# Kernel optimization log

Measured on AMD Instinct MI355X. Metric: run time of the kernel, lower is better.

Reference implementation:

```python
import jax, jax.numpy as jnp
import numpy as np


def setup_inputs() -> dict:
    key = jax.random.key(0)
    kx, kwi, kwh = jax.random.split(key, 3)
    B, T, F, H = 32, 2048, 512, 512
    x = jax.random.normal(kx, (B, T, F), dtype=jnp.float32)
    c0 = jnp.zeros((B, H), dtype=jnp.float32)
    h0 = jnp.zeros((B, H), dtype=jnp.float32)
    # Flax OptimizedLSTMCell: fused kernels, gates in (i, f, g, o) order.
    # Input projection has no bias; recurrent projection carries the bias.
    Wi = jax.random.normal(kwi, (F, 4 * H), dtype=jnp.float32) / np.sqrt(F)
    Wh = jax.random.normal(kwh, (H, 4 * H), dtype=jnp.float32) / np.sqrt(H)
    b = jnp.zeros((4 * H,), dtype=jnp.float32)
    return {"x": x, "c0": c0, "h0": h0, "Wi": Wi, "Wh": Wh, "b": b}


def reference(x, c0, h0, Wi, Wh, b):
    # x: [B, T, F]; scan over time (axis 1), matching nn.scan(in_axes=1, out_axes=1).
    def step(carry, xt):
        c, h = carry
        z = xt @ Wi + h @ Wh + b  # [B, 4H]
        i, f, g, o = jnp.split(z, 4, axis=-1)
        i = jax.nn.sigmoid(i)
        f = jax.nn.sigmoid(f)
        g = jnp.tanh(g)
        o = jax.nn.sigmoid(o)
        c_new = f * c + i * g
        h_new = o * jnp.tanh(c_new)
        return (c_new, h_new), h_new

    xs = jnp.swapaxes(x, 0, 1)  # [T, B, F]
    (c_fin, h_fin), ys = jax.lax.scan(step, (c0, h0), xs)
    ys = jnp.swapaxes(ys, 0, 1)  # [B, T, H]
    return (c_fin, h_fin), ys
```

## Files before the change

### kernel.cpp

```cpp
#include <hip/hip_runtime.h>
#include <hip/hip_bf16.h>

#define B_    32
#define T_    2048
#define F_    512
#define H_    512
#define G_    64
#define NCOL  32
#define WPITCH 520
#define SLOT  (B_ * H_)
#define DSL   64

typedef __attribute__((ext_vector_type(8))) short short8;
typedef __attribute__((ext_vector_type(4))) float floatx4;

static __device__ __forceinline__ short bf16s(float f) {
    return __builtin_bit_cast(short, __float2bfloat16(f));
}
__device__ __forceinline__ float sigmoidf_(float x) {
    return 1.0f / (1.0f + __expf(-x));
}

__global__ void prep_kernel(const float* __restrict__ x,
                            const float* __restrict__ h0,
                            unsigned short* __restrict__ xb,
                            unsigned short* __restrict__ h_slot_last,
                            int do_x)
{
    const int tid = threadIdx.x;
    if (blockIdx.x < 64) {
        const int idx = blockIdx.x * 256 + tid;
        h_slot_last[idx] = (unsigned short)bf16s(h0[idx]);
        return;
    }
    if (!do_x) return;
    const long long base = ((long long)(blockIdx.x - 64) * 256 + tid) * 8;
    const floatx4 a = *(const floatx4*)(x + base);
    const floatx4 b = *(const floatx4*)(x + base + 4);
    short8 s;
    s[0] = bf16s(a[0]); s[1] = bf16s(a[1]); s[2] = bf16s(a[2]); s[3] = bf16s(a[3]);
    s[4] = bf16s(b[0]); s[5] = bf16s(b[1]); s[6] = bf16s(b[2]); s[7] = bf16s(b[3]);
    *(short8*)(xb + base) = s;
}

template<bool XB>
__global__ __launch_bounds__(256, 1)
void lstm_loop(const float* __restrict__ x,
               const unsigned short* __restrict__ xb,
               const float* __restrict__ c0,
               const float* __restrict__ Wi,
               const float* __restrict__ Wh,
               const float* __restrict__ bias,
               float* __restrict__ out,
               unsigned short* __restrict__ hbuf,
               unsigned int* __restrict__ flags)
{
    __shared__ short wtI[NCOL][WPITCH];
    __shared__ short wtH[NCOL][WPITCH];
    __shared__ float zbuf[B_][NCOL + 1];
    __shared__ __align__(16) unsigned short h_lds[B_][8];

    const int tid = threadIdx.x;
    const int wg  = blockIdx.x;

    for (int idx = tid; idx < NCOL * F_; idx += 256) {
        const int j  = idx & (NCOL - 1);
        const int k  = idx >> 5;
        const int gi = j >> 3, hc = j & 7;
        const int gcol = gi * H_ + wg * 8 + hc;
        wtI[j][k] = bf16s(Wi[k * (4 * H_) + gcol]);
        wtH[j][k] = bf16s(Wh[k * (4 * H_) + gcol]);
    }

    const int gb    = tid >> 3;
    const int ghc   = tid & 7;
    const int hglob = wg * 8 + ghc;
    float c_val  = c0[gb * H_ + hglob];
    float h_last = 0.f;
    const float bi = bias[0 * H_ + hglob];
    const float bf = bias[1 * H_ + hglob];
    const float bg = bias[2 * H_ + hglob];
    const float bo = bias[3 * H_ + hglob];

    const int wid  = tid >> 6;
    const int lane = tid & 63;
    const int mt   = wid >> 1;
    const int nt   = wid & 1;
    const int ln   = lane & 15;
    const int lq   = lane >> 4;
    const int arow = mt * 16 + ln;

    float* ys = out + 2 * B_ * H_;

    __syncthreads();

    for (int t = 0; t < T_; ++t) {
        floatx4 accx = {0.f, 0.f, 0.f, 0.f};
        if (XB) {
            const unsigned short* xrow = xb + (arow * T_ + t) * F_;
            #pragma unroll
            for (int ks = 0; ks < 16; ++ks) {
                const int koff = ks * 32 + lq * 8;
                const short8 ax = *(const short8*)(xrow + koff);
                const short8 bx = *(const short8*)&wtI[nt * 16 + ln][koff];
                accx = __builtin_amdgcn_mfma_f32_16x16x32_bf16(ax, bx, accx, 0, 0, 0);
            }
        } else {
            const float* xrow = x + (arow * T_ + t) * F_;
            #pragma unroll
            for (int ks = 0; ks < 16; ++ks) {
                const int koff = ks * 32 + lq * 8;
                const floatx4 xa = *(const floatx4*)(xrow + koff);
                const floatx4 xc = *(const floatx4*)(xrow + koff + 4);
                short8 ax;
                ax[0] = bf16s(xa[0]); ax[1] = bf16s(xa[1]);
                ax[2] = bf16s(xa[2]); ax[3] = bf16s(xa[3]);
                ax[4] = bf16s(xc[0]); ax[5] = bf16s(xc[1]);
                ax[6] = bf16s(xc[2]); ax[7] = bf16s(xc[3]);
                const short8 bx = *(const short8*)&wtI[nt * 16 + ln][koff];
                accx = __builtin_amdgcn_mfma_f32_16x16x32_bf16(ax, bx, accx, 0, 0, 0);
            }
        }

        if (t > 0) {
            if (wid == 0) {
                int spins = 0;
                while (true) {
                    const unsigned f = __hip_atomic_load(&flags[lane], __ATOMIC_RELAXED,
                                                         __HIP_MEMORY_SCOPE_AGENT);
                    if (__all((int)(f >= (unsigned)t))) break;
                    if (++spins > (1 << 16)) break;
                }
            }
            __syncthreads();
            if ((t & (DSL - 1)) == 0)
                __builtin_amdgcn_fence(__ATOMIC_ACQUIRE, "agent");
        }

        const unsigned short* hrow = hbuf + ((t - 1) & (DSL - 1)) * SLOT + arow * H_;
        floatx4 acch = {0.f, 0.f, 0.f, 0.f};
        #pragma unroll
        for (int ks = 0; ks < 16; ++ks) {
            const int koff = ks * 32 + lq * 8;
            const short8 ah = *(const short8*)(hrow + koff);
            const short8 bh = *(const short8*)&wtH[nt * 16 + ln][koff];
            acch = __builtin_amdgcn_mfma_f32_16x16x32_bf16(ah, bh, acch, 0, 0, 0);
        }
        {
            const int zrow = mt * 16 + lq * 4;
            const int zcol = nt * 16 + ln;
            #pragma unroll
            for (int r = 0; r < 4; ++r)
                zbuf[zrow + r][zcol] = accx[r] + acch[r];
        }
        __syncthreads();

        {
            const float zi = zbuf[gb][ghc]       + bi;
            const float zf = zbuf[gb][8  + ghc]  + bf;
            const float zg = zbuf[gb][16 + ghc]  + bg;
            const float zo = zbuf[gb][24 + ghc]  + bo;
            const float ig = sigmoidf_(zi);
            const float fg = sigmoidf_(zf);
            const float gg = tanhf(zg);
            const float og = sigmoidf_(zo);
            c_val  = fg * c_val + ig * gg;
            h_last = og * tanhf(c_val);
            h_lds[gb][ghc] = (unsigned short)bf16s(h_last);
            ys[(gb * T_ + t) * H_ + hglob] = h_last;
        }
        __syncthreads();

        if (tid < 64) {
            const int row = tid >> 1, c4 = (tid & 1) * 4;
            const unsigned long long v = *(const unsigned long long*)&h_lds[row][c4];
            __hip_atomic_store((unsigned long long*)(hbuf + (t & (DSL - 1)) * SLOT
                                                     + row * H_ + wg * 8 + c4),
                               v, __ATOMIC_RELAXED, __HIP_MEMORY_SCOPE_AGENT);
        }
        __syncthreads();
        if (tid == 0)
            __hip_atomic_store(&flags[wg], (unsigned)(t + 1), __ATOMIC_RELAXED,
                               __HIP_MEMORY_SCOPE_AGENT);
    }

    out[gb * H_ + hglob]           = c_val;
    out[B_ * H_ + gb * H_ + hglob] = h_last;
}

extern "C" void kernel_launch(void* const* d_in, const int* in_sizes, int n_in,
                              void* d_out, int out_size, void* d_ws, size_t ws_size,
                              hipStream_t stream) {
    const float* x  = (const float*)d_in[0];
    const float* c0 = (const float*)d_in[1];
    const float* h0 = (const float*)d_in[2];
    const float* Wi = (const float*)d_in[3];
    const float* Wh = (const float*)d_in[4];
    const float* b  = (const float*)d_in[5];
    float* out = (float*)d_out;

    unsigned char* ws = (unsigned char*)d_ws;
    unsigned int*   flags = (unsigned int*)ws;
    unsigned short* hbuf  = (unsigned short*)(ws + 65536);
    unsigned short* xb    = (unsigned short*)(ws + 65536 + (size_t)DSL * SLOT * 2);

    const size_t need_xb = 65536 + (size_t)DSL * SLOT * 2 + (size_t)B_ * T_ * F_ * 2;
    const int use_xb = (ws_size >= need_xb) ? 1 : 0;

    hipMemsetAsync(ws, 0, 4096, stream);

    const int prep_blocks = 64 + (use_xb ? (B_ * T_ * F_ / 8 / 256) : 0);
    prep_kernel<<<prep_blocks, 256, 0, stream>>>(x, h0, xb, hbuf + (DSL - 1) * SLOT, use_xb);

    void* args[] = { &x, &xb, &c0, &Wi, &Wh, &b, &out, &hbuf, &flags };
    hipLaunchCooperativeKernel(use_xb ? (void*)lstm_loop<true> : (void*)lstm_loop<false>,
                               dim3(G_), dim3(256), args, 0, stream);
}
```

Before: 10.28 ms.

## Replace flag-based grid barrier with tagged hidden-state ring polled per load

Removes the per-step flag array and the wave-0 spin barrier. Each hidden value is now stored as a 32-bit word with the timestep tag in its upper half, written directly from every thread into a 4-slot ring. Consumers issue cache-bypassing loads of their h fragments and re-poll only the chunks whose tags do not yet match, so synchronisation happens at fine granularity and overlaps with the recurrent MFMA loop. It also drops two __syncthreads and the LDS staging of h per step. In exchange, h traffic doubles in width, the code relies on inline-asm sc0 sc1 loads for coherence, and a small 4-slot ring risks slot reuse before slow readers finish (the spin cap silently proceeds).

```diff
diff --git a/kernel.cpp b/kernel.cpp
--- a/kernel.cpp
+++ b/kernel.cpp
@@ -8,29 +8,59 @@
 #define G_    64
 #define NCOL  32
 #define WPITCH 520
-#define SLOT  (B_ * H_)
-#define DSL   64
+#define BH    (B_ * H_)
+#define DSL   4
 
 typedef __attribute__((ext_vector_type(8))) short short8;
 typedef __attribute__((ext_vector_type(4))) float floatx4;
-
-static __device__ __forceinline__ short bf16s(float f) {
-    return __builtin_bit_cast(short, __float2bfloat16(f));
+typedef __attribute__((ext_vector_type(4))) unsigned int uint4v;
+
+static __device__ __forceinline__ unsigned short bf16u(float f) {
+    return (unsigned short)__builtin_bit_cast(short, __float2bfloat16(f));
 }
 __device__ __forceinline__ float sigmoidf_(float x) {
     return 1.0f / (1.0f + __expf(-x));
+}
+
+#define ISSUE2(w0_, w1_, p_)                                                 \
+    asm volatile("global_load_dwordx4 %0, %2, off sc0 sc1\n\t"               \
+                 "global_load_dwordx4 %1, %3, off sc0 sc1"                   \
+                 : "=&v"(w0_), "=&v"(w1_)                                    \
+                 : "v"(p_), "v"((p_) + 4) : "memory")
+#define REISSUE2(w0_, w1_, p_)                                               \
+    asm volatile("global_load_dwordx4 %0, %2, off sc0 sc1\n\t"               \
+                 "global_load_dwordx4 %1, %3, off sc0 sc1\n\t"               \
+                 "s_waitcnt vmcnt(0)"                                        \
+                 : "=&v"(w0_), "=&v"(w1_)                                    \
+                 : "v"(p_), "v"((p_) + 4) : "memory")
+#define WAITV(n) asm volatile("s_waitcnt vmcnt(" #n ")" ::: "memory")
+
+__device__ __forceinline__ bool tagok(uint4v a, uint4v b, unsigned tg) {
+    unsigned m = ((a.x >> 16) ^ tg) | ((a.y >> 16) ^ tg) |
+                 ((a.z >> 16) ^ tg) | ((a.w >> 16) ^ tg) |
+                 ((b.x >> 16) ^ tg) | ((b.y >> 16) ^ tg) |
+                 ((b.z >> 16) ^ tg) | ((b.w >> 16) ^ tg);
+    return m == 0;
+}
+__device__ __forceinline__ short8 unpack8(uint4v a, uint4v b) {
+    short8 r;
+    r[0] = (short)a.x; r[1] = (short)a.y; r[2] = (short)a.z; r[3] = (short)a.w;
+    r[4] = (short)b.x; r[5] = (short)b.y; r[6] = (short)b.z; r[7] = (short)b.w;
+    return r;
 }
 
 __global__ void prep_kernel(const float* __restrict__ x,
                             const float* __restrict__ h0,
                             unsigned short* __restrict__ xb,
-                            unsigned short* __restrict__ h_slot_last,
+                            unsigned int* __restrict__ ring,
                             int do_x)
 {
     const int tid = threadIdx.x;
     if (blockIdx.x < 64) {
         const int idx = blockIdx.x * 256 + tid;
-        h_slot_last[idx] = (unsigned short)bf16s(h0[idx]);
+        const unsigned v = (0xFFFFu << 16) | (unsigned)bf16u(h0[idx]);
+        __hip_atomic_store(&ring[(DSL - 1) * BH + idx], v,
+                           __ATOMIC_RELAXED, __HIP_MEMORY_SCOPE_AGENT);
         return;
     }
     if (!do_x) return;
@@ -38,8 +68,10 @@
     const floatx4 a = *(const floatx4*)(x + base);
     const floatx4 b = *(const floatx4*)(x + base + 4);
     short8 s;
-    s[0] = bf16s(a[0]); s[1] = bf16s(a[1]); s[2] = bf16s(a[2]); s[3] = bf16s(a[3]);
-    s[4] = bf16s(b[0]); s[5] = bf16s(b[1]); s[6] = bf16s(b[2]); s[7] = bf16s(b[3]);
+    s[0] = (short)bf16u(a[0]); s[1] = (short)bf16u(a[1]);
+    s[2] = (short)bf16u(a[2]); s[3] = (short)bf16u(a[3]);
+    s[4] = (short)bf16u(b[0]); s[5] = (short)bf16u(b[1]);
+    s[6] = (short)bf16u(b[2]); s[7] = (short)bf16u(b[3]);
     *(short8*)(xb + base) = s;
 }
 
@@ -52,13 +84,11 @@
                const float* __restrict__ Wh,
                const float* __restrict__ bias,
                float* __restrict__ out,
-               unsigned short* __restrict__ hbuf,
-               unsigned int* __restrict__ flags)
+               unsigned int* __restrict__ ring)
 {
     __shared__ short wtI[NCOL][WPITCH];
     __shared__ short wtH[NCOL][WPITCH];
     __shared__ float zbuf[B_][NCOL + 1];
-    __shared__ __align__(16) unsigned short h_lds[B_][8];
 
     const int tid = threadIdx.x;
     const int wg  = blockIdx.x;
@@ -68,8 +98,8 @@
         const int k  = idx >> 5;
         const int gi = j >> 3, hc = j & 7;
         const int gcol = gi * H_ + wg * 8 + hc;
-        wtI[j][k] = bf16s(Wi[k * (4 * H_) + gcol]);
-        wtH[j][k] = bf16s(Wh[k * (4 * H_) + gcol]);
+        wtI[j][k] = (short)bf16u(Wi[k * (4 * H_) + gcol]);
+        wtH[j][k] = (short)bf16u(Wh[k * (4 * H_) + gcol]);
     }
 
     const int gb    = tid >> 3;
@@ -113,39 +143,44 @@
                 const floatx4 xa = *(const floatx4*)(xrow + koff);
                 const floatx4 xc = *(const floatx4*)(xrow + koff + 4);
                 short8 ax;
-                ax[0] = bf16s(xa[0]); ax[1] = bf16s(xa[1]);
-                ax[2] = bf16s(xa[2]); ax[3] = bf16s(xa[3]);
-                ax[4] = bf16s(xc[0]); ax[5] = bf16s(xc[1]);
-                ax[6] = bf16s(xc[2]); ax[7] = bf16s(xc[3]);
+                ax[0] = (short)bf16u(xa[0]); ax[1] = (short)bf16u(xa[1]);
+                ax[2] = (short)bf16u(xa[2]); ax[3] = (short)bf16u(xa[3]);
+                ax[4] = (short)bf16u(xc[0]); ax[5] = (short)bf16u(xc[1]);
+                ax[6] = (short)bf16u(xc[2]); ax[7] = (short)bf16u(xc[3]);
                 const short8 bx = *(const short8*)&wtI[nt * 16 + ln][koff];
                 accx = __builtin_amdgcn_mfma_f32_16x16x32_bf16(ax, bx, accx, 0, 0, 0);
             }
         }
 
-        if (t > 0) {
-            if (wid == 0) {
-                int spins = 0;
-                while (true) {
-                    const unsigned f = __hip_atomic_load(&flags[lane], __ATOMIC_RELAXED,
-                                                         __HIP_MEMORY_SCOPE_AGENT);
-                    if (__all((int)(f >= (unsigned)t))) break;
-                    if (++spins > (1 << 16)) break;
-                }
-            }
-            __syncthreads();
-            if ((t & (DSL - 1)) == 0)
-                __builtin_amdgcn_fence(__ATOMIC_ACQUIRE, "agent");
-        }
-
-        const unsigned short* hrow = hbuf + ((t - 1) & (DSL - 1)) * SLOT + arow * H_;
+        const unsigned int* hslot = ring + ((t - 1) & (DSL - 1)) * BH + arow * H_ + lq * 8;
+        const unsigned tg = (unsigned)((t - 1) & 0xFFFF);
         floatx4 acch = {0.f, 0.f, 0.f, 0.f};
+        uint4v wa[4], wb[4];
+
+        #pragma unroll
+        for (int g = 0; g < 4; ++g) { ISSUE2(wa[g], wb[g], hslot + g * 32); }
+
         #pragma unroll
         for (int ks = 0; ks < 16; ++ks) {
-            const int koff = ks * 32 + lq * 8;
-            const short8 ah = *(const short8*)(hrow + koff);
-            const short8 bh = *(const short8*)&wtH[nt * 16 + ln][koff];
+            if (ks <= 12)      { WAITV(6); }
+            else if (ks == 13) { WAITV(4); }
+            else if (ks == 14) { WAITV(2); }
+            else               { WAITV(0); }
+
+            const int slot4 = ks & 3;
+            if (!tagok(wa[slot4], wb[slot4], tg)) {
+                int spins = 0;
+                do {
+                    REISSUE2(wa[slot4], wb[slot4], hslot + ks * 32);
+                } while (!tagok(wa[slot4], wb[slot4], tg) && ++spins < (1 << 13));
+            }
+            const short8 ah = unpack8(wa[slot4], wb[slot4]);
+            if (ks + 4 < 16) { ISSUE2(wa[slot4], wb[slot4], hslot + (ks + 4) * 32); }
+
+            const short8 bh = *(const short8*)&wtH[nt * 16 + ln][ks * 32 + lq * 8];
             acch = __builtin_amdgcn_mfma_f32_16x16x32_bf16(ah, bh, acch, 0, 0, 0);
         }
+
         {
             const int zrow = mt * 16 + lq * 4;
             const int zcol = nt * 16 + ln;
@@ -166,22 +201,12 @@
             const float og = sigmoidf_(zo);
             c_val  = fg * c_val + ig * gg;
             h_last = og * tanhf(c_val);
-            h_lds[gb][ghc] = (unsigned short)bf16s(h_last);
+            const unsigned v = ((unsigned)(t & 0xFFFF) << 16) | (unsigned)bf16u(h_last);
+            __hip_atomic_store(&ring[(t & (DSL - 1)) * BH + gb * H_ + hglob], v,
+                               __ATOMIC_RELAXED, __HIP_MEMORY_SCOPE_AGENT);
             ys[(gb * T_ + t) * H_ + hglob] = h_last;
         }
         __syncthreads();
-
-        if (tid < 64) {
-            const int row = tid >> 1, c4 = (tid & 1) * 4;
-            const unsigned long long v = *(const unsigned long long*)&h_lds[row][c4];
-            __hip_atomic_store((unsigned long long*)(hbuf + (t & (DSL - 1)) * SLOT
-                                                     + row * H_ + wg * 8 + c4),
-                               v, __ATOMIC_RELAXED, __HIP_MEMORY_SCOPE_AGENT);
-        }
-        __syncthreads();
-        if (tid == 0)
-            __hip_atomic_store(&flags[wg], (unsigned)(t + 1), __ATOMIC_RELAXED,
-                               __HIP_MEMORY_SCOPE_AGENT);
     }
 
     out[gb * H_ + hglob]           = c_val;
@@ -200,19 +225,16 @@
     float* out = (float*)d_out;
 
     unsigned char* ws = (unsigned char*)d_ws;
-    unsigned int*   flags = (unsigned int*)ws;
-    unsigned short* hbuf  = (unsigned short*)(ws + 65536);
-    unsigned short* xb    = (unsigned short*)(ws + 65536 + (size_t)DSL * SLOT * 2);
-
-    const size_t need_xb = 65536 + (size_t)DSL * SLOT * 2 + (size_t)B_ * T_ * F_ * 2;
+    unsigned int*   ring = (unsigned int*)ws;
+    unsigned short* xb   = (unsigned short*)(ws + (size_t)DSL * BH * 4);
+
+    const size_t need_xb = (size_t)DSL * BH * 4 + (size_t)B_ * T_ * F_ * 2;
     const int use_xb = (ws_size >= need_xb) ? 1 : 0;
 
-    hipMemsetAsync(ws, 0, 4096, stream);
-
     const int prep_blocks = 64 + (use_xb ? (B_ * T_ * F_ / 8 / 256) : 0);
-    prep_kernel<<<prep_blocks, 256, 0, stream>>>(x, h0, xb, hbuf + (DSL - 1) * SLOT, use_xb);
-
-    void* args[] = { &x, &xb, &c0, &Wi, &Wh, &b, &out, &hbuf, &flags };
+    prep_kernel<<<prep_blocks, 256, 0, stream>>>(x, h0, xb, ring, use_xb);
+
+    void* args[] = { &x, &xb, &c0, &Wi, &Wh, &b, &out, &ring };
     hipLaunchCooperativeKernel(use_xb ? (void*)lstm_loop<true> : (void*)lstm_loop<false>,
                                dim3(G_), dim3(256), args, 0, stream);
 }
```

After: 15.17 ms. 1.48x slower.
